# Optimization experiments

Measured on AMD Instinct MI355X. Metric: run time of the kernel, lower is better.

Reference implementation:

```python
import jax, jax.numpy as jnp
import numpy as np

B, S, H = 4, 2048, 1024
NH, HD = 16, 64


def setup_inputs() -> dict:
    key = jax.random.key(0)
    ks = jax.random.split(key, 5)
    scale = 1.0 / np.sqrt(H)
    x = jax.random.normal(ks[0], (B, S, H), dtype=jnp.float32)
    w_qkv = jax.random.normal(ks[1], (H, 3 * H), dtype=jnp.float32) * scale
    b_qkv = jnp.zeros((3 * H,), dtype=jnp.float32)
    w_out = jax.random.normal(ks[2], (H, H), dtype=jnp.float32) * scale
    b_out = jnp.zeros((H,), dtype=jnp.float32)
    return {"x": x, "w_qkv": w_qkv, "b_qkv": b_qkv, "w_out": w_out, "b_out": b_out}


def reference(x, w_qkv, b_qkv, w_out, b_out):
    bsz, seq_len, hidden = x.shape
    qkv = x @ w_qkv + b_qkv  # [B,S,3H]
    q, k, v = jnp.split(qkv, 3, axis=-1)

    def heads(t):
        return t.reshape(bsz, seq_len, NH, HD).transpose(0, 2, 1, 3)  # [B,NH,S,HD]

    q, k, v = heads(q), heads(k), heads(v)
    scale = HD ** (-0.5)
    attn = jnp.einsum("bhqd,bhkd->bhqk", q, k) * scale  # [B,NH,S,S]
    causal = jnp.tril(jnp.ones((seq_len, seq_len), dtype=bool))
    attn = jnp.where(causal, attn, -jnp.inf)
    probs = jax.nn.softmax(attn, axis=-1)
    out = jnp.einsum("bhqk,bhkd->bhqd", probs, v)
    out = out.transpose(0, 2, 1, 3).reshape(bsz, seq_len, hidden)
    return out @ w_out + b_out
```

## Files before the change

### kernel.cpp

```cpp
#include <hip/hip_runtime.h>
#include <hip/hip_bf16.h>
#include <cstdint>

#define B_  4
#define S_  2048
#define H_  1024
#define NH_ 16
#define HD_ 64

using short8  = __attribute__((ext_vector_type(8))) short;
using floatx4 = __attribute__((ext_vector_type(4))) float;

__device__ __forceinline__ unsigned short f2b(float f) {
  union { float f; unsigned int u; } x; x.f = f;
  unsigned int r = x.u + 0x7fffu + ((x.u >> 16) & 1u);
  return (unsigned short)(r >> 16);
}
__device__ __forceinline__ unsigned short f2b_fast(float f) {
  union { float f; unsigned int u; } x; x.f = f;
  return (unsigned short)((x.u + 0x8000u) >> 16);
}
__device__ __forceinline__ unsigned int pack2(float a, float b) {
  return (unsigned int)f2b(a) | ((unsigned int)f2b(b) << 16);
}

__device__ __forceinline__ void async16(void* lds, const void* g) {
  __builtin_amdgcn_global_load_lds(
      (const __attribute__((address_space(1))) unsigned int*)g,
      (__attribute__((address_space(3))) unsigned int*)lds, 16, 0, 0);
}

__device__ __forceinline__ void transpose_tile(const float* __restrict__ in,
                                               unsigned short* __restrict__ out,
                                               int R, int C, int c0, int r0) {
  __shared__ float tile[32][33];
  int tx = threadIdx.x & 31, ty = threadIdx.x >> 5;
  for (int i = 0; i < 4; i++) {
    int r = r0 + ty + i * 8;
    tile[ty + i * 8][tx] = in[(size_t)r * C + c0 + tx];
  }
  __syncthreads();
  for (int i = 0; i < 4; i++) {
    int c = c0 + ty + i * 8;
    out[(size_t)c * R + r0 + tx] = f2b(tile[tx][ty + i * 8]);
  }
}

__global__ void k_prep(const float* __restrict__ x, const float* __restrict__ w_qkv,
                       const float* __restrict__ w_out,
                       unsigned short* __restrict__ xb, unsigned short* __restrict__ wqkvT,
                       unsigned short* __restrict__ woutT) {
  int bx = blockIdx.x;
  if (bx < 8192) {
    int i = (bx * 256 + threadIdx.x) * 4;
    float4 v = *(const float4*)(x + i);
    ushort4 o;
    o.x = f2b(v.x); o.y = f2b(v.y); o.z = f2b(v.z); o.w = f2b(v.w);
    *(ushort4*)(xb + i) = o;
  } else if (bx < 8192 + 3072) {
    int t = bx - 8192;
    transpose_tile(w_qkv, wqkvT, H_, 3 * H_, (t % 96) * 32, (t / 96) * 32);
  } else {
    int t = bx - 8192 - 3072;
    transpose_tile(w_out, woutT, H_, H_, (t & 31) * 32, (t >> 5) * 32);
  }
}

template <bool OUT_BF16>
__global__ __launch_bounds__(256, 4) void k_gemm_bt(
    const unsigned short* __restrict__ A,
    const unsigned short* __restrict__ BT,
    const float* __restrict__ bias,
    void* __restrict__ Cout,
    unsigned short* __restrict__ vt,
    int M, int N, int K) {
  __shared__ __align__(16) unsigned short As[2][128 * 32];
  __shared__ __align__(16) unsigned short Bs[2][128 * 32];
  const int tid  = threadIdx.x;
  const int lane = tid & 63, wave = tid >> 6;
  const int quad = lane >> 4, l16 = lane & 15;
  const int wm = wave >> 1, wn = wave & 1;
  const int m0 = blockIdx.y * 128, n0 = blockIdx.x * 128;
  const int wv2 = wave & 1;

  const unsigned short* srcbase = (wave < 2) ? A : BT;
  const int base0 = (wave < 2) ? m0 : n0;

  floatx4 acc[4][4];
  for (int mt = 0; mt < 4; mt++)
    for (int nt = 0; nt < 4; nt++)
      acc[mt][nt] = (floatx4){0.f, 0.f, 0.f, 0.f};

  auto stage = [&](int k0, int bufi) {
    unsigned short* dst = (wave < 2) ? &As[bufi][0] : &Bs[bufi][0];
    for (int j = 0; j < 4; j++) {
      int c = wv2 * 256 + j * 64 + lane;
      int row = c >> 2, slot = c & 3;
      int c8 = slot ^ ((row >> 1) & 3);
      async16(&dst[c * 8], &srcbase[(size_t)(base0 + row) * K + k0 + c8 * 8]);
    }
  };

  stage(0, 0);
  int it = 0;
  for (int k0 = 0; k0 < K; k0 += 32, it++) {
    const int cur = it & 1;
    __syncthreads();
    if (k0 + 32 < K) stage(k0 + 32, cur ^ 1);
    short8 af[4], bq[4];
    for (int t = 0; t < 4; t++) {
      int ra = wm * 64 + t * 16 + l16;
      int rb = wn * 64 + t * 16 + l16;
      af[t] = *(const short8*)&As[cur][(ra * 4 + (quad ^ ((ra >> 1) & 3))) * 8];
      bq[t] = *(const short8*)&Bs[cur][(rb * 4 + (quad ^ ((rb >> 1) & 3))) * 8];
    }
    for (int mt = 0; mt < 4; mt++)
      for (int nt = 0; nt < 4; nt++)
        acc[mt][nt] = __builtin_amdgcn_mfma_f32_16x16x32_bf16(af[mt], bq[nt], acc[mt][nt], 0, 0, 0);
  }

  if (OUT_BF16 && n0 >= 2048) {
    for (int mt = 0; mt < 4; mt++) {
      int row0 = m0 + wm * 64 + mt * 16 + quad * 4;
      int b = row0 >> 11, s = row0 & 2047;
      for (int nt = 0; nt < 4; nt++) {
        int col = n0 + wn * 64 + nt * 16 + l16;
        float bv = bias[col];
        uint2 u;
        u.x = pack2(acc[mt][nt][0] + bv, acc[mt][nt][1] + bv);
        u.y = pack2(acc[mt][nt][2] + bv, acc[mt][nt][3] + bv);
        *(uint2*)&vt[(size_t)(b * 1024 + (col - 2048)) * S_ + s] = u;
      }
    }
  } else {
    for (int mt = 0; mt < 4; mt++) {
      int row = m0 + wm * 64 + mt * 16 + quad * 4;
      for (int nt = 0; nt < 4; nt++) {
        int col = n0 + wn * 64 + nt * 16 + l16;
        float bv = bias[col];
        for (int r = 0; r < 4; r++) {
          float v = acc[mt][nt][r] + bv;
          if (OUT_BF16) ((unsigned short*)Cout)[(size_t)(row + r) * N + col] = f2b(v);
          else          ((float*)Cout)[(size_t)(row + r) * N + col] = v;
        }
      }
    }
  }
}

__global__ __launch_bounds__(256, 3) void k_attn(
    const unsigned short* __restrict__ qkv,
    const unsigned short* __restrict__ vt,
    unsigned short* __restrict__ outb) {
  __shared__ __align__(16) unsigned short Ks [2][64 * 64];
  __shared__ __align__(16) unsigned short VTs[2][64 * 64];
  __shared__ __align__(16) unsigned short Ps[4][16 * 64];

  const int tid  = threadIdx.x;
  const int lane = tid & 63, w = tid >> 6;
  const int quad = lane >> 4, l16 = lane & 15;
  const int qt = (S_ / 128 - 1) - (blockIdx.x >> 6);
  const int bh = blockIdx.x & 63;
  const int b = bh >> 4, h = bh & 15;
  const int qwv = qt * 128 + w * 32;
  const int wv2 = w & 1;

  short8 qf[2][2];
  for (int g = 0; g < 2; g++)
    for (int kh = 0; kh < 2; kh++)
      qf[g][kh] = *(const short8*)&qkv[(size_t)(b * S_ + qwv + g * 16 + l16) * (3 * H_)
                                       + h * HD_ + kh * 32 + quad * 8];

  floatx4 oacc[2][4];
  float lsum[2] = {0.f, 0.f};
  for (int g = 0; g < 2; g++)
    for (int ct = 0; ct < 4; ct++) oacc[g][ct] = (floatx4){0.f, 0.f, 0.f, 0.f};

  auto stage = [&](int kt, int bufi) {
    if (w < 2) {
      for (int j = 0; j < 4; j++) {
        int c = wv2 * 256 + j * 64 + lane;
        int row = c >> 3, c8 = (c & 7) ^ (row & 7);
        async16(&Ks[bufi][c * 8],
                &qkv[(size_t)(b * S_ + kt * 64 + row) * (3 * H_) + H_ + h * HD_ + c8 * 8]);
      }
    } else {
      for (int j = 0; j < 4; j++) {
        int c = wv2 * 256 + j * 64 + lane;
        int row = c >> 3, c8 = (c & 7) ^ (row & 7);
        async16(&VTs[bufi][c * 8],
                &vt[(size_t)(bh * HD_ + row) * S_ + kt * 64 + c8 * 8]);
      }
    }
  };

  unsigned short* Pw = &Ps[w][0];

  const int ktmax = 2 * qt + 1;
  stage(0, 0);
  for (int kt = 0; kt <= ktmax; kt++) {
    const int cur = kt & 1;
    __syncthreads();
    if (kt < ktmax) stage(kt + 1, cur ^ 1);

    if (kt * 64 <= qwv + 31) {
      const bool need_mask = (kt * 64 + 63 > qwv);

      short8 vf[4][2];
      for (int ct = 0; ct < 4; ct++)
        for (int kh = 0; kh < 2; kh++) {
          int vrow = ct * 16 + l16;
          vf[ct][kh] = *(const short8*)&VTs[cur][(vrow * 8 + ((kh * 4 + quad) ^ (vrow & 7))) * 8];
        }

      uint2 pk[2][4];
      for (int ct = 0; ct < 4; ct++) {
        int krow = ct * 16 + l16;
        short8 kf0 = *(const short8*)&Ks[cur][(krow * 8 + ((0 + quad) ^ (krow & 7))) * 8];
        short8 kf1 = *(const short8*)&Ks[cur][(krow * 8 + ((4 + quad) ^ (krow & 7))) * 8];
        for (int g = 0; g < 2; g++) {
          floatx4 z = (floatx4){0.f, 0.f, 0.f, 0.f};
          z = __builtin_amdgcn_mfma_f32_16x16x32_bf16(kf0, qf[g][0], z, 0, 0, 0);
          z = __builtin_amdgcn_mfma_f32_16x16x32_bf16(kf1, qf[g][1], z, 0, 0, 0);
          float p[4];
          if (need_mask) {
            int kvb = kt * 64 + ct * 16 + quad * 4;
            int q = qwv + g * 16 + l16;
            for (int r = 0; r < 4; r++)
              p[r] = (kvb + r <= q) ? __expf(z[r] * 0.125f) : 0.f;
          } else {
            for (int r = 0; r < 4; r++) p[r] = __expf(z[r] * 0.125f);
          }
          lsum[g] += (p[0] + p[1]) + (p[2] + p[3]);
          pk[g][ct].x = (unsigned int)f2b_fast(p[0]) | ((unsigned int)f2b_fast(p[1]) << 16);
          pk[g][ct].y = (unsigned int)f2b_fast(p[2]) | ((unsigned int)f2b_fast(p[3]) << 16);
        }
      }

      for (int g = 0; g < 2; g++) {
        for (int ct = 0; ct < 4; ct++) {
          int slot = (ct * 2 + (quad >> 1)) ^ (l16 & 7);
          *(uint2*)&Pw[l16 * 64 + slot * 8 + (quad & 1) * 4] = pk[g][ct];
        }
        for (int kh = 0; kh < 2; kh++) {
          short8 pf = *(const short8*)&Pw[l16 * 64 + ((kh * 4 + quad) ^ (l16 & 7)) * 8];
          for (int ct = 0; ct < 4; ct++)
            oacc[g][ct] = __builtin_amdgcn_mfma_f32_16x16x32_bf16(vf[ct][kh], pf, oacc[g][ct], 0, 0, 0);
        }
      }
    }
  }

  for (int g = 0; g < 2; g++) {
    lsum[g] += __shfl_xor(lsum[g], 16);
    lsum[g] += __shfl_xor(lsum[g], 32);
  }

  for (int g = 0; g < 2; g++) {
    float inv = 1.0f / lsum[g];
    int q = qwv + g * 16 + l16;
    for (int ct = 0; ct < 4; ct++) {
      uint2 u;
      u.x = pack2(oacc[g][ct][0] * inv, oacc[g][ct][1] * inv);
      u.y = pack2(oacc[g][ct][2] * inv, oacc[g][ct][3] * inv);
      *(uint2*)&outb[(size_t)(b * S_ + q) * H_ + h * HD_ + ct * 16 + quad * 4] = u;
    }
  }
}

extern "C" void kernel_launch(void* const* d_in, const int* in_sizes, int n_in,
                              void* d_out, int out_size, void* d_ws, size_t ws_size,
                              hipStream_t stream) {
  const float* x     = (const float*)d_in[0];
  const float* w_qkv = (const float*)d_in[1];
  const float* b_qkv = (const float*)d_in[2];
  const float* w_out = (const float*)d_in[3];
  const float* b_out = (const float*)d_in[4];

  char* ws = (char*)d_ws;
  size_t off = 0;
  auto alloc = [&](size_t bytes) -> void* {
    void* p = ws + off;
    off = (off + bytes + 255) & ~(size_t)255;
    return p;
  };
  unsigned short* xb    = (unsigned short*)alloc((size_t)B_ * S_ * H_ * 2);
  unsigned short* wqkvT = (unsigned short*)alloc((size_t)3 * H_ * H_ * 2);
  unsigned short* woutT = (unsigned short*)alloc((size_t)H_ * H_ * 2);
  unsigned short* qkv   = (unsigned short*)alloc((size_t)B_ * S_ * 3 * H_ * 2);
  unsigned short* ao    = (unsigned short*)alloc((size_t)B_ * S_ * H_ * 2);
  unsigned short* vtb   = (unsigned short*)alloc((size_t)B_ * NH_ * HD_ * S_ * 2);

  k_prep<<<8192 + 3072 + 1024, 256, 0, stream>>>(x, w_qkv, w_out, xb, wqkvT, woutT);

  k_gemm_bt<true ><<<dim3(3 * H_ / 128, B_ * S_ / 128), 256, 0, stream>>>(
      xb, wqkvT, b_qkv, qkv, vtb, B_ * S_, 3 * H_, H_);

  k_attn<<<(S_ / 128) * 64, 256, 0, stream>>>(qkv, vtb, ao);

  k_gemm_bt<false><<<dim3(H_ / 128, B_ * S_ / 128), 256, 0, stream>>>(
      ao, woutT, b_out, (float*)d_out, nullptr, B_ * S_, H_, H_);
}
```

Measured before the change: 246.3 us.

## Rewrite GEMMs as 8-wave 256x128 tiles with triple-buffered K=64 pipeline

Replaces the 4-wave 128x128 double-buffered GEMM with an 8-wave kernel. It computes 256x128 output tiles using K=64 slices, triple-buffered LDS and a 3-bit XOR swizzle. The main loop splits each K step into two MFMA phases, interleaving A prefetch halves with explicit s_barrier, waitcnt and setprio scheduling so loads overlap compute. This costs much more LDS (~144KB per block) and lower occupancy, and the hand-placed vmcnt counts must exactly match the issued loads.

```diff
diff --git a/kernel.cpp b/kernel.cpp
--- a/kernel.cpp
+++ b/kernel.cpp
@@ -67,62 +67,120 @@
 }
 
 template <bool OUT_BF16>
-__global__ __launch_bounds__(256, 4) void k_gemm_bt(
+__global__ __launch_bounds__(512, 2) void k_gemm8(
     const unsigned short* __restrict__ A,
     const unsigned short* __restrict__ BT,
     const float* __restrict__ bias,
     void* __restrict__ Cout,
     unsigned short* __restrict__ vt,
     int M, int N, int K) {
-  __shared__ __align__(16) unsigned short As[2][128 * 32];
-  __shared__ __align__(16) unsigned short Bs[2][128 * 32];
+  __shared__ __align__(16) unsigned short As[3][256 * 64];
+  __shared__ __align__(16) unsigned short Bs[3][128 * 64];
   const int tid  = threadIdx.x;
   const int lane = tid & 63, wave = tid >> 6;
   const int quad = lane >> 4, l16 = lane & 15;
   const int wm = wave >> 1, wn = wave & 1;
-  const int m0 = blockIdx.y * 128, n0 = blockIdx.x * 128;
-  const int wv2 = wave & 1;
-
-  const unsigned short* srcbase = (wave < 2) ? A : BT;
-  const int base0 = (wave < 2) ? m0 : n0;
+  const int m0 = blockIdx.y * 256, n0 = blockIdx.x * 128;
+  const int NT = K >> 6;
 
   floatx4 acc[4][4];
+#pragma unroll
   for (int mt = 0; mt < 4; mt++)
+#pragma unroll
     for (int nt = 0; nt < 4; nt++)
       acc[mt][nt] = (floatx4){0.f, 0.f, 0.f, 0.f};
 
-  auto stage = [&](int k0, int bufi) {
-    unsigned short* dst = (wave < 2) ? &As[bufi][0] : &Bs[bufi][0];
-    for (int j = 0; j < 4; j++) {
-      int c = wv2 * 256 + j * 64 + lane;
-      int row = c >> 2, slot = c & 3;
-      int c8 = slot ^ ((row >> 1) & 3);
-      async16(&dst[c * 8], &srcbase[(size_t)(base0 + row) * K + k0 + c8 * 8]);
+  auto stageA = [&](int kt, int bi, int half) {
+#pragma unroll
+    for (int j = 0; j < 2; j++) {
+      int c = half * 1024 + j * 512 + tid;
+      int row = c >> 3, c8 = (c & 7) ^ (row & 7);
+      async16(&As[bi][c * 8], &A[(size_t)(m0 + row) * K + kt * 64 + c8 * 8]);
     }
   };
-
-  stage(0, 0);
-  int it = 0;
-  for (int k0 = 0; k0 < K; k0 += 32, it++) {
-    const int cur = it & 1;
-    __syncthreads();
-    if (k0 + 32 < K) stage(k0 + 32, cur ^ 1);
-    short8 af[4], bq[4];
-    for (int t = 0; t < 4; t++) {
-      int ra = wm * 64 + t * 16 + l16;
-      int rb = wn * 64 + t * 16 + l16;
-      af[t] = *(const short8*)&As[cur][(ra * 4 + (quad ^ ((ra >> 1) & 3))) * 8];
-      bq[t] = *(const short8*)&Bs[cur][(rb * 4 + (quad ^ ((rb >> 1) & 3))) * 8];
-    }
-    for (int mt = 0; mt < 4; mt++)
-      for (int nt = 0; nt < 4; nt++)
-        acc[mt][nt] = __builtin_amdgcn_mfma_f32_16x16x32_bf16(af[mt], bq[nt], acc[mt][nt], 0, 0, 0);
+  auto stageB = [&](int kt, int bi) {
+#pragma unroll
+    for (int j = 0; j < 2; j++) {
+      int c = j * 512 + tid;
+      int row = c >> 3, c8 = (c & 7) ^ (row & 7);
+      async16(&Bs[bi][c * 8], &BT[(size_t)(n0 + row) * K + kt * 64 + c8 * 8]);
+    }
+  };
+
+  stageA(0, 0, 0); stageA(0, 0, 1); stageB(0, 0);
+  stageA(1, 1, 0); stageA(1, 1, 1); stageB(1, 1);
+  asm volatile("s_waitcnt vmcnt(6)" ::: "memory");
+  __builtin_amdgcn_s_barrier();
+
+  int buf = 0;
+  for (int kt = 0; kt < NT; kt++) {
+    const int bn = (buf >= 1) ? buf - 1 : 2;
+    const bool pf = (kt + 2 < NT);
+
+    if (pf) { stageA(kt + 2, bn, 0); stageB(kt + 2, bn); }
+    short8 bq[4][2], af[2][2];
+#pragma unroll
+    for (int nt = 0; nt < 4; nt++) {
+      int rb = wn * 64 + nt * 16 + l16;
+#pragma unroll
+      for (int ks = 0; ks < 2; ks++)
+        bq[nt][ks] = *(const short8*)&Bs[buf][(rb * 8 + ((ks * 4 + quad) ^ (rb & 7))) * 8];
+    }
+#pragma unroll
+    for (int mt = 0; mt < 2; mt++) {
+      int ra = wm * 64 + mt * 16 + l16;
+#pragma unroll
+      for (int ks = 0; ks < 2; ks++)
+        af[mt][ks] = *(const short8*)&As[buf][(ra * 8 + ((ks * 4 + quad) ^ (ra & 7))) * 8];
+    }
+    __builtin_amdgcn_s_barrier();
+    asm volatile("s_waitcnt lgkmcnt(0)" ::: "memory");
+    __builtin_amdgcn_sched_barrier(0);
+    __builtin_amdgcn_s_setprio(1);
+#pragma unroll
+    for (int ks = 0; ks < 2; ks++)
+#pragma unroll
+      for (int mt = 0; mt < 2; mt++)
+#pragma unroll
+        for (int nt = 0; nt < 4; nt++)
+          acc[mt][nt] = __builtin_amdgcn_mfma_f32_16x16x32_bf16(af[mt][ks], bq[nt][ks], acc[mt][nt], 0, 0, 0);
+    __builtin_amdgcn_s_setprio(0);
+    __builtin_amdgcn_s_barrier();
+
+    if (pf) stageA(kt + 2, bn, 1);
+#pragma unroll
+    for (int mt = 0; mt < 2; mt++) {
+      int ra = wm * 64 + (2 + mt) * 16 + l16;
+#pragma unroll
+      for (int ks = 0; ks < 2; ks++)
+        af[mt][ks] = *(const short8*)&As[buf][(ra * 8 + ((ks * 4 + quad) ^ (ra & 7))) * 8];
+    }
+    __builtin_amdgcn_s_barrier();
+    asm volatile("s_waitcnt lgkmcnt(0)" ::: "memory");
+    __builtin_amdgcn_sched_barrier(0);
+    __builtin_amdgcn_s_setprio(1);
+#pragma unroll
+    for (int ks = 0; ks < 2; ks++)
+#pragma unroll
+      for (int mt = 0; mt < 2; mt++)
+#pragma unroll
+        for (int nt = 0; nt < 4; nt++)
+          acc[2 + mt][nt] = __builtin_amdgcn_mfma_f32_16x16x32_bf16(af[mt][ks], bq[nt][ks], acc[2 + mt][nt], 0, 0, 0);
+    __builtin_amdgcn_s_setprio(0);
+    if (kt + 1 < NT) {
+      if (pf) asm volatile("s_waitcnt vmcnt(6)" ::: "memory");
+      else    asm volatile("s_waitcnt vmcnt(0)" ::: "memory");
+    }
+    __builtin_amdgcn_s_barrier();
+    buf = (buf == 2) ? 0 : buf + 1;
   }
 
   if (OUT_BF16 && n0 >= 2048) {
+#pragma unroll
     for (int mt = 0; mt < 4; mt++) {
       int row0 = m0 + wm * 64 + mt * 16 + quad * 4;
       int b = row0 >> 11, s = row0 & 2047;
+#pragma unroll
       for (int nt = 0; nt < 4; nt++) {
         int col = n0 + wn * 64 + nt * 16 + l16;
         float bv = bias[col];
@@ -133,11 +191,14 @@
       }
     }
   } else {
+#pragma unroll
     for (int mt = 0; mt < 4; mt++) {
       int row = m0 + wm * 64 + mt * 16 + quad * 4;
+#pragma unroll
       for (int nt = 0; nt < 4; nt++) {
         int col = n0 + wn * 64 + nt * 16 + l16;
         float bv = bias[col];
+#pragma unroll
         for (int r = 0; r < 4; r++) {
           float v = acc[mt][nt][r] + bv;
           if (OUT_BF16) ((unsigned short*)Cout)[(size_t)(row + r) * N + col] = f2b(v);
@@ -293,11 +354,11 @@
 
   k_prep<<<8192 + 3072 + 1024, 256, 0, stream>>>(x, w_qkv, w_out, xb, wqkvT, woutT);
 
-  k_gemm_bt<true ><<<dim3(3 * H_ / 128, B_ * S_ / 128), 256, 0, stream>>>(
+  k_gemm8<true ><<<dim3(3 * H_ / 128, B_ * S_ / 256), 512, 0, stream>>>(
       xb, wqkvT, b_qkv, qkv, vtb, B_ * S_, 3 * H_, H_);
 
   k_attn<<<(S_ / 128) * 64, 256, 0, stream>>>(qkv, vtb, ao);
 
-  k_gemm_bt<false><<<dim3(H_ / 128, B_ * S_ / 128), 256, 0, stream>>>(
+  k_gemm8<false><<<dim3(H_ / 128, B_ * S_ / 256), 512, 0, stream>>>(
       ao, woutT, b_out, (float*)d_out, nullptr, B_ * S_, H_, H_);
 }
```

Result: slower. 279.8 us (+13.6%).

## Add 256x256-tile, 512-thread QKV GEMM with 4-stage async pipeline

Applied to the files above, without the earlier changes.

Replaces the 128x128 QKV projection GEMM with a new kernel that uses 256x256 output tiles, 8 waves and a 4-deep async LDS buffer ring with prefetch distance 3. Each k-step is split into two MFMA halves, with barriers and raised wave priority to interleave loads and compute. The larger tile is meant to raise operand reuse per global load and hide memory latency. In exchange it uses 128KB of LDS and more accumulator registers per thread. The grid also drops to 12x32 blocks, which may underfill the GPU's compute units.

```diff
diff --git a/kernel.cpp b/kernel.cpp
--- a/kernel.cpp
+++ b/kernel.cpp
@@ -63,6 +63,140 @@
   } else {
     int t = bx - 8192 - 3072;
     transpose_tile(w_out, woutT, H_, H_, (t & 31) * 32, (t >> 5) * 32);
+  }
+}
+
+template <bool OUT_BF16>
+__global__ __launch_bounds__(512, 2) void k_gemm256(
+    const unsigned short* __restrict__ A,
+    const unsigned short* __restrict__ BT,
+    const float* __restrict__ bias,
+    void* __restrict__ Cout,
+    unsigned short* __restrict__ vt,
+    int M, int N, int K) {
+  __shared__ __align__(16) unsigned short As[4][256 * 32];
+  __shared__ __align__(16) unsigned short Bs[4][256 * 32];
+  const int tid  = threadIdx.x;
+  const int lane = tid & 63, wave = tid >> 6;
+  const int quad = lane >> 4, l16 = lane & 15;
+  const int wm = wave >> 2, wn = wave & 3;
+  const int m0 = blockIdx.y * 256, n0 = blockIdx.x * 256;
+  const int NT = K >> 5;
+
+  floatx4 acc[8][4];
+#pragma unroll
+  for (int mt = 0; mt < 8; mt++)
+#pragma unroll
+    for (int nt = 0; nt < 4; nt++)
+      acc[mt][nt] = (floatx4){0.f, 0.f, 0.f, 0.f};
+
+  auto stageA = [&](int t) {
+    unsigned short* dst = &As[t & 3][0];
+#pragma unroll
+    for (int j = 0; j < 2; j++) {
+      int c = j * 512 + tid;
+      int row = c >> 2, c8 = (c & 3) ^ ((row >> 1) & 3);
+      async16(&dst[c * 8], &A[(size_t)(m0 + row) * K + t * 32 + c8 * 8]);
+    }
+  };
+  auto stageB = [&](int t) {
+    unsigned short* dst = &Bs[t & 3][0];
+#pragma unroll
+    for (int j = 0; j < 2; j++) {
+      int c = j * 512 + tid;
+      int row = c >> 2, c8 = (c & 3) ^ ((row >> 1) & 3);
+      async16(&dst[c * 8], &BT[(size_t)(n0 + row) * K + t * 32 + c8 * 8]);
+    }
+  };
+
+  stageA(0); stageB(0); stageA(1); stageB(1); stageA(2); stageB(2);
+  asm volatile("s_waitcnt vmcnt(8)" ::: "memory");
+  __builtin_amdgcn_s_barrier();
+
+  for (int t = 0; t < NT; t++) {
+    const int bi = t & 3;
+    const bool pf = (t + 3 < NT);
+
+    if (pf) stageA(t + 3);
+    short8 bq[4], af[4];
+#pragma unroll
+    for (int nt = 0; nt < 4; nt++) {
+      int rb = wn * 64 + nt * 16 + l16;
+      bq[nt] = *(const short8*)&Bs[bi][(rb * 4 + (quad ^ ((rb >> 1) & 3))) * 8];
+    }
+#pragma unroll
+    for (int mt = 0; mt < 4; mt++) {
+      int ra = wm * 128 + mt * 16 + l16;
+      af[mt] = *(const short8*)&As[bi][(ra * 4 + (quad ^ ((ra >> 1) & 3))) * 8];
+    }
+    __builtin_amdgcn_s_barrier();
+    asm volatile("s_waitcnt lgkmcnt(0)" ::: "memory");
+    __builtin_amdgcn_sched_barrier(0);
+    __builtin_amdgcn_s_setprio(1);
+#pragma unroll
+    for (int mt = 0; mt < 4; mt++)
+#pragma unroll
+      for (int nt = 0; nt < 4; nt++)
+        acc[mt][nt] = __builtin_amdgcn_mfma_f32_16x16x32_bf16(af[mt], bq[nt], acc[mt][nt], 0, 0, 0);
+    __builtin_amdgcn_s_setprio(0);
+    __builtin_amdgcn_s_barrier();
+
+    if (pf) stageB(t + 3);
+#pragma unroll
+    for (int mt = 0; mt < 4; mt++) {
+      int ra = wm * 128 + (4 + mt) * 16 + l16;
+      af[mt] = *(const short8*)&As[bi][(ra * 4 + (quad ^ ((ra >> 1) & 3))) * 8];
+    }
+    __builtin_amdgcn_s_barrier();
+    asm volatile("s_waitcnt lgkmcnt(0)" ::: "memory");
+    __builtin_amdgcn_sched_barrier(0);
+    __builtin_amdgcn_s_setprio(1);
+#pragma unroll
+    for (int mt = 0; mt < 4; mt++)
+#pragma unroll
+      for (int nt = 0; nt < 4; nt++)
+        acc[4 + mt][nt] = __builtin_amdgcn_mfma_f32_16x16x32_bf16(af[mt], bq[nt], acc[4 + mt][nt], 0, 0, 0);
+    __builtin_amdgcn_s_setprio(0);
+
+    if (t + 1 < NT) {
+      if (pf)                 asm volatile("s_waitcnt vmcnt(8)" ::: "memory");
+      else if (t + 2 < NT)    asm volatile("s_waitcnt vmcnt(4)" ::: "memory");
+      else                    asm volatile("s_waitcnt vmcnt(0)" ::: "memory");
+      __builtin_amdgcn_s_barrier();
+    }
+  }
+
+  if (OUT_BF16 && n0 >= 2048) {
+#pragma unroll
+    for (int mt = 0; mt < 8; mt++) {
+      int row0 = m0 + wm * 128 + mt * 16 + quad * 4;
+      int b = row0 >> 11, s = row0 & 2047;
+#pragma unroll
+      for (int nt = 0; nt < 4; nt++) {
+        int col = n0 + wn * 64 + nt * 16 + l16;
+        float bv = bias[col];
+        uint2 u;
+        u.x = pack2(acc[mt][nt][0] + bv, acc[mt][nt][1] + bv);
+        u.y = pack2(acc[mt][nt][2] + bv, acc[mt][nt][3] + bv);
+        *(uint2*)&vt[(size_t)(b * 1024 + (col - 2048)) * S_ + s] = u;
+      }
+    }
+  } else {
+#pragma unroll
+    for (int mt = 0; mt < 8; mt++) {
+      int row = m0 + wm * 128 + mt * 16 + quad * 4;
+#pragma unroll
+      for (int nt = 0; nt < 4; nt++) {
+        int col = n0 + wn * 64 + nt * 16 + l16;
+        float bv = bias[col];
+#pragma unroll
+        for (int r = 0; r < 4; r++) {
+          float v = acc[mt][nt][r] + bv;
+          if (OUT_BF16) ((unsigned short*)Cout)[(size_t)(row + r) * N + col] = f2b(v);
+          else          ((float*)Cout)[(size_t)(row + r) * N + col] = v;
+        }
+      }
+    }
   }
 }
 
@@ -293,7 +427,7 @@
 
   k_prep<<<8192 + 3072 + 1024, 256, 0, stream>>>(x, w_qkv, w_out, xb, wqkvT, woutT);
 
-  k_gemm_bt<true ><<<dim3(3 * H_ / 128, B_ * S_ / 128), 256, 0, stream>>>(
+  k_gemm256<true ><<<dim3(3 * H_ / 256, B_ * S_ / 256), 512, 0, stream>>>(
       xb, wqkvT, b_qkv, qkv, vtb, B_ * S_, 3 * H_, H_);
 
   k_attn<<<(S_ / 128) * 64, 256, 0, stream>>>(qkv, vtb, ao);
```

After: 283.9 us. 1.15x slower.

## Deepen GEMM K-tile to 64 and fold softmax scale into Q weights

Applied to the files above, without the earlier changes.

The GEMM kernel now stages 64-wide K slices per iteration, using 8-chunk XOR-swizzled LDS layouts and issuing both A and B loads from all waves. This halves the barrier and loop count per GEMM and raises MFMA work per sync, at the cost of doubled LDS and a lower occupancy hint (2 blocks per CU). Separately, the 1/sqrt(HD) factor is pre-multiplied into the Q columns of the QKV weights and bias, so the attention kernel no longer multiplies each score before exp. Scaling before bf16 rounding is exact because 0.125 is a power of two.

```diff
diff --git a/kernel.cpp b/kernel.cpp
--- a/kernel.cpp
+++ b/kernel.cpp
@@ -32,7 +32,8 @@
 
 __device__ __forceinline__ void transpose_tile(const float* __restrict__ in,
                                                unsigned short* __restrict__ out,
-                                               int R, int C, int c0, int r0) {
+                                               int R, int C, int c0, int r0,
+                                               bool qk_scale) {
   __shared__ float tile[32][33];
   int tx = threadIdx.x & 31, ty = threadIdx.x >> 5;
   for (int i = 0; i < 4; i++) {
@@ -42,7 +43,8 @@
   __syncthreads();
   for (int i = 0; i < 4; i++) {
     int c = c0 + ty + i * 8;
-    out[(size_t)c * R + r0 + tx] = f2b(tile[tx][ty + i * 8]);
+    float s = (qk_scale && c < 1024) ? 0.125f : 1.0f;
+    out[(size_t)c * R + r0 + tx] = f2b(tile[tx][ty + i * 8] * s);
   }
 }
 
@@ -59,70 +61,83 @@
     *(ushort4*)(xb + i) = o;
   } else if (bx < 8192 + 3072) {
     int t = bx - 8192;
-    transpose_tile(w_qkv, wqkvT, H_, 3 * H_, (t % 96) * 32, (t / 96) * 32);
+    transpose_tile(w_qkv, wqkvT, H_, 3 * H_, (t % 96) * 32, (t / 96) * 32, true);
   } else {
     int t = bx - 8192 - 3072;
-    transpose_tile(w_out, woutT, H_, H_, (t & 31) * 32, (t >> 5) * 32);
+    transpose_tile(w_out, woutT, H_, H_, (t & 31) * 32, (t >> 5) * 32, false);
   }
 }
 
 template <bool OUT_BF16>
-__global__ __launch_bounds__(256, 4) void k_gemm_bt(
+__global__ __launch_bounds__(256, 2) void k_gemm_bt64(
     const unsigned short* __restrict__ A,
     const unsigned short* __restrict__ BT,
     const float* __restrict__ bias,
     void* __restrict__ Cout,
     unsigned short* __restrict__ vt,
     int M, int N, int K) {
-  __shared__ __align__(16) unsigned short As[2][128 * 32];
-  __shared__ __align__(16) unsigned short Bs[2][128 * 32];
+  __shared__ __align__(16) unsigned short As[2][128 * 64];
+  __shared__ __align__(16) unsigned short Bs[2][128 * 64];
   const int tid  = threadIdx.x;
   const int lane = tid & 63, wave = tid >> 6;
   const int quad = lane >> 4, l16 = lane & 15;
   const int wm = wave >> 1, wn = wave & 1;
   const int m0 = blockIdx.y * 128, n0 = blockIdx.x * 128;
-  const int wv2 = wave & 1;
-
-  const unsigned short* srcbase = (wave < 2) ? A : BT;
-  const int base0 = (wave < 2) ? m0 : n0;
 
   floatx4 acc[4][4];
+#pragma unroll
   for (int mt = 0; mt < 4; mt++)
+#pragma unroll
     for (int nt = 0; nt < 4; nt++)
       acc[mt][nt] = (floatx4){0.f, 0.f, 0.f, 0.f};
 
   auto stage = [&](int k0, int bufi) {
-    unsigned short* dst = (wave < 2) ? &As[bufi][0] : &Bs[bufi][0];
+#pragma unroll
     for (int j = 0; j < 4; j++) {
-      int c = wv2 * 256 + j * 64 + lane;
-      int row = c >> 2, slot = c & 3;
-      int c8 = slot ^ ((row >> 1) & 3);
-      async16(&dst[c * 8], &srcbase[(size_t)(base0 + row) * K + k0 + c8 * 8]);
+      int c = j * 256 + tid;
+      int row = c >> 3, c8 = (c & 7) ^ (row & 7);
+      async16(&As[bufi][c * 8], &A[(size_t)(m0 + row) * K + k0 + c8 * 8]);
+    }
+#pragma unroll
+    for (int j = 0; j < 4; j++) {
+      int c = j * 256 + tid;
+      int row = c >> 3, c8 = (c & 7) ^ (row & 7);
+      async16(&Bs[bufi][c * 8], &BT[(size_t)(n0 + row) * K + k0 + c8 * 8]);
     }
   };
 
   stage(0, 0);
   int it = 0;
-  for (int k0 = 0; k0 < K; k0 += 32, it++) {
+  for (int k0 = 0; k0 < K; k0 += 64, it++) {
     const int cur = it & 1;
     __syncthreads();
-    if (k0 + 32 < K) stage(k0 + 32, cur ^ 1);
-    short8 af[4], bq[4];
+    if (k0 + 64 < K) stage(k0 + 64, cur ^ 1);
+    short8 af[4][2], bq[4][2];
+#pragma unroll
     for (int t = 0; t < 4; t++) {
       int ra = wm * 64 + t * 16 + l16;
       int rb = wn * 64 + t * 16 + l16;
-      af[t] = *(const short8*)&As[cur][(ra * 4 + (quad ^ ((ra >> 1) & 3))) * 8];
-      bq[t] = *(const short8*)&Bs[cur][(rb * 4 + (quad ^ ((rb >> 1) & 3))) * 8];
-    }
-    for (int mt = 0; mt < 4; mt++)
-      for (int nt = 0; nt < 4; nt++)
-        acc[mt][nt] = __builtin_amdgcn_mfma_f32_16x16x32_bf16(af[mt], bq[nt], acc[mt][nt], 0, 0, 0);
+#pragma unroll
+      for (int ks = 0; ks < 2; ks++) {
+        af[t][ks] = *(const short8*)&As[cur][(ra * 8 + ((ks * 4 + quad) ^ (ra & 7))) * 8];
+        bq[t][ks] = *(const short8*)&Bs[cur][(rb * 8 + ((ks * 4 + quad) ^ (rb & 7))) * 8];
+      }
+    }
+#pragma unroll
+    for (int ks = 0; ks < 2; ks++)
+#pragma unroll
+      for (int mt = 0; mt < 4; mt++)
+#pragma unroll
+        for (int nt = 0; nt < 4; nt++)
+          acc[mt][nt] = __builtin_amdgcn_mfma_f32_16x16x32_bf16(af[mt][ks], bq[nt][ks], acc[mt][nt], 0, 0, 0);
   }
 
   if (OUT_BF16 && n0 >= 2048) {
+#pragma unroll
     for (int mt = 0; mt < 4; mt++) {
       int row0 = m0 + wm * 64 + mt * 16 + quad * 4;
       int b = row0 >> 11, s = row0 & 2047;
+#pragma unroll
       for (int nt = 0; nt < 4; nt++) {
         int col = n0 + wn * 64 + nt * 16 + l16;
         float bv = bias[col];
@@ -133,11 +148,15 @@
       }
     }
   } else {
+#pragma unroll
     for (int mt = 0; mt < 4; mt++) {
       int row = m0 + wm * 64 + mt * 16 + quad * 4;
+#pragma unroll
       for (int nt = 0; nt < 4; nt++) {
         int col = n0 + wn * 64 + nt * 16 + l16;
         float bv = bias[col];
+        if (OUT_BF16 && col < 1024) bv *= 0.125f;
+#pragma unroll
         for (int r = 0; r < 4; r++) {
           float v = acc[mt][nt][r] + bv;
           if (OUT_BF16) ((unsigned short*)Cout)[(size_t)(row + r) * N + col] = f2b(v);
@@ -227,9 +246,9 @@
             int kvb = kt * 64 + ct * 16 + quad * 4;
             int q = qwv + g * 16 + l16;
             for (int r = 0; r < 4; r++)
-              p[r] = (kvb + r <= q) ? __expf(z[r] * 0.125f) : 0.f;
+              p[r] = (kvb + r <= q) ? __expf(z[r]) : 0.f;
           } else {
-            for (int r = 0; r < 4; r++) p[r] = __expf(z[r] * 0.125f);
+            for (int r = 0; r < 4; r++) p[r] = __expf(z[r]);
           }
           lsum[g] += (p[0] + p[1]) + (p[2] + p[3]);
           pk[g][ct].x = (unsigned int)f2b_fast(p[0]) | ((unsigned int)f2b_fast(p[1]) << 16);
@@ -293,11 +312,11 @@
 
   k_prep<<<8192 + 3072 + 1024, 256, 0, stream>>>(x, w_qkv, w_out, xb, wqkvT, woutT);
 
-  k_gemm_bt<true ><<<dim3(3 * H_ / 128, B_ * S_ / 128), 256, 0, stream>>>(
+  k_gemm_bt64<true ><<<dim3(3 * H_ / 128, B_ * S_ / 128), 256, 0, stream>>>(
       xb, wqkvT, b_qkv, qkv, vtb, B_ * S_, 3 * H_, H_);
 
   k_attn<<<(S_ / 128) * 64, 256, 0, stream>>>(qkv, vtb, ao);
 
-  k_gemm_bt<false><<<dim3(H_ / 128, B_ * S_ / 128), 256, 0, stream>>>(
+  k_gemm_bt64<false><<<dim3(H_ / 128, B_ * S_ / 128), 256, 0, stream>>>(
       ao, woutT, b_out, (float*)d_out, nullptr, B_ * S_, H_, H_);
 }
```

New measurement: 243.4 us (median of 2 runs). No clear change (-1.2%).
